# Kernel tuning notes

Measured on AMD Instinct MI355X. Metric: run time of the kernel, lower is better.

## Reference

```python
import jax, jax.numpy as jnp
import numpy as np

B, T, D, H = 32, 1024, 256, 256


def setup_inputs() -> dict:
    key = jax.random.key(0)
    ks = jax.random.split(key, 11)
    x = jax.random.normal(ks[0], (B, T, D), dtype=jnp.float32)
    len_x = jax.random.randint(ks[1], (B,), 1, T + 1).astype(jnp.int32)

    def xavier(k, fan_in, fan_out):
        return (jax.random.normal(k, (fan_out, fan_in)) * np.sqrt(2.0 / (fan_in + fan_out))).astype(jnp.float32)

    def unif(k, fan_in, shape):
        bound = 1.0 / np.sqrt(fan_in)
        return jax.random.uniform(k, shape, minval=-bound, maxval=bound).astype(jnp.float32)

    return {
        "x": x, "len_x": len_x,
        "Ww1_w": xavier(ks[2], D, H), "Ww1_b": unif(ks[3], D, (H,)),
        "Ww2_w": unif(ks[4], H, (D, H)), "Ww2_b": unif(ks[5], H, (D,)),
        "Wb1_w": xavier(ks[6], D, H), "Wb1_b": unif(ks[7], D, (H,)),
        "Wb2_w": unif(ks[8], H, (D, H)), "Wb2_b": unif(ks[9], H, (D,)),
    }


def _mlp(c, w1, b1, w2, b2):
    h = jax.nn.gelu(c @ w1.T + b1, approximate=False)
    return h @ w2.T + b2


def _ragged_dft(z, lengths, inverse):
    # z: [B, T, D] complex64; per-sample DFT over the first lengths[i] steps.
    t = z.shape[1]
    n = jnp.arange(t)
    kn = (n[:, None] * n[None, :]).astype(jnp.float32)          # [T, T]
    l = lengths.astype(jnp.float32)[:, None, None]               # [B, 1, 1]
    sign = 1.0 if inverse else -1.0
    ang = sign * 2.0 * jnp.pi * kn[None, :, :] / l               # [B, T, T]
    valid = n[None, :] < lengths[:, None]                        # [B, T]
    mask = (valid[:, :, None] & valid[:, None, :]).astype(jnp.float32)
    Wm = jnp.exp(1j * ang).astype(jnp.complex64) * mask
    if inverse:
        Wm = Wm / l.astype(jnp.complex64)
    return jnp.einsum("bkn,bnd->bkd", Wm, z)


def _crelu(z):
    mag = jnp.abs(z)
    phase = jnp.angle(z)
    recomposed = (mag * jnp.exp(1j * phase)).astype(jnp.complex64)
    return jnp.where(mag > 0, recomposed, jnp.zeros((), jnp.complex64))


def reference(x, len_x, Ww1_w, Ww1_b, Ww2_w, Ww2_b, Wb1_w, Wb1_b, Wb2_w, Wb2_b):
    # mean over valid length (torch sums over full T; padding assumed zero-filled contributes)
    c = jnp.sum(x, axis=1) / len_x.astype(x.dtype)[:, None]      # [B, D]
    x_freq = _ragged_dft(x.astype(jnp.complex64), len_x, inverse=False)
    W = _mlp(c, Ww1_w, Ww1_b, Ww2_w, Ww2_b).astype(jnp.complex64)  # [B, D]
    b = _mlp(c, Wb1_w, Wb1_b, Wb2_w, Wb2_b).astype(jnp.complex64)  # [B, D]
    filtered = x_freq * (1.0 + W[:, None, :]) + b[:, None, :]
    activated = _crelu(filtered)
    x_recon = _ragged_dft(activated, len_x, inverse=True)
    return x_recon.real.astype(x.dtype)
```

## Files before the change

### kernel.cpp

```cpp
#include <hip/hip_runtime.h>
#include <math.h>

#define BB 32
#define TT 1024
#define DD 256
#define NCHUNK 16
#define TCH (TT / NCHUNK)

__global__ void k_partial(const float* __restrict__ x, float* __restrict__ partial) {
    int blk = blockIdx.x;
    int b   = blk / NCHUNK;
    int ch  = blk % NCHUNK;
    int d   = threadIdx.x;
    const float* px = x + ((size_t)b * TT + (size_t)ch * TCH) * DD + d;
    float s = 0.f;
#pragma unroll 8
    for (int t = 0; t < TCH; ++t) s += px[(size_t)t * DD];
    partial[(b * NCHUNK + ch) * DD + d] = s;
}

__global__ void k_cfinal(const float* __restrict__ partial, const int* __restrict__ len,
                         float* __restrict__ c) {
    int b = blockIdx.x;
    int d = threadIdx.x;
    float s = 0.f;
#pragma unroll
    for (int ch = 0; ch < NCHUNK; ++ch) s += partial[(b * NCHUNK + ch) * DD + d];
    c[b * DD + d] = s / (float)len[b];
}

__device__ __forceinline__ float wave_reduce(float s) {
#pragma unroll
    for (int off = 32; off; off >>= 1) s += __shfl_xor(s, off, 64);
    return s;
}

__global__ void k_layer1(const float* __restrict__ c,
                         const float* __restrict__ w1a, const float* __restrict__ b1a,
                         const float* __restrict__ w1b, const float* __restrict__ b1b,
                         float* __restrict__ h) {
    int gwave = (blockIdx.x * blockDim.x + threadIdx.x) >> 6;
    int lane  = threadIdx.x & 63;
    int mlp   = gwave >> 8;
    int j     = gwave & 255;
    const float* w1 = mlp ? w1b : w1a;
    const float* b1 = mlp ? b1b : b1a;
    float4 wr  = ((const float4*)(w1 + j * DD))[lane];
    float bias = b1[j];
    for (int b = 0; b < BB; ++b) {
        float4 cc = ((const float4*)(c + b * DD))[lane];
        float s = wr.x * cc.x + wr.y * cc.y + wr.z * cc.z + wr.w * cc.w;
        s = wave_reduce(s);
        if (lane == 0) {
            float v = s + bias;
            float g = 0.5f * v * (1.0f + erff(v * 0.70710678118654752440f));
            h[(mlp * BB + b) * DD + j] = g;
        }
    }
}

__global__ void k_layer2(const float* __restrict__ h,
                         const float* __restrict__ w2a, const float* __restrict__ b2a,
                         const float* __restrict__ w2b, const float* __restrict__ b2b,
                         float* __restrict__ Wout, float* __restrict__ Bout) {
    int gwave = (blockIdx.x * blockDim.x + threadIdx.x) >> 6;
    int lane  = threadIdx.x & 63;
    int mlp   = gwave >> 8;
    int d     = gwave & 255;
    const float* w2 = mlp ? w2b : w2a;
    const float* b2 = mlp ? b2b : b2a;
    float* outp = mlp ? Bout : Wout;
    float4 wr  = ((const float4*)(w2 + d * DD))[lane];
    float bias = b2[d];
    const float* hbase = h + mlp * BB * DD;
    for (int b = 0; b < BB; ++b) {
        float4 hh = ((const float4*)(hbase + b * DD))[lane];
        float s = wr.x * hh.x + wr.y * hh.y + wr.z * hh.z + wr.w * hh.w;
        s = wave_reduce(s);
        if (lane == 0) outp[b * DD + d] = s + bias;
    }
}

__global__ void k_apply(const float* __restrict__ x, const int* __restrict__ len,
                        const float* __restrict__ Wf, const float* __restrict__ Bf,
                        float* __restrict__ out) {
    int row  = blockIdx.x * 4 + (threadIdx.x >> 6);
    int lane = threadIdx.x & 63;
    int b = row >> 10;
    int t = row & 1023;
    int L = len[b];
    size_t base = (size_t)row * DD;
    float4* o4 = (float4*)(out + base);
    if (t >= L) {
        float4 z; z.x = 0.f; z.y = 0.f; z.z = 0.f; z.w = 0.f;
        o4[lane] = z;
        return;
    }
    float4 x4 = ((const float4*)(x + base))[lane];
    float4 w4 = ((const float4*)(Wf + b * DD))[lane];
    float4 r;
    r.x = x4.x + w4.x * x4.x;
    r.y = x4.y + w4.y * x4.y;
    r.z = x4.z + w4.z * x4.z;
    r.w = x4.w + w4.w * x4.w;
    if (t == 0) {
        float4 b4 = ((const float4*)(Bf + b * DD))[lane];
        r.x += b4.x; r.y += b4.y; r.z += b4.z; r.w += b4.w;
    }
    o4[lane] = r;
}

extern "C" void kernel_launch(void* const* d_in, const int* in_sizes, int n_in,
                              void* d_out, int out_size, void* d_ws, size_t ws_size,
                              hipStream_t stream) {
    const float* x     = (const float*)d_in[0];
    const int*   len   = (const int*)d_in[1];
    const float* Ww1_w = (const float*)d_in[2];
    const float* Ww1_b = (const float*)d_in[3];
    const float* Ww2_w = (const float*)d_in[4];
    const float* Ww2_b = (const float*)d_in[5];
    const float* Wb1_w = (const float*)d_in[6];
    const float* Wb1_b = (const float*)d_in[7];
    const float* Wb2_w = (const float*)d_in[8];
    const float* Wb2_b = (const float*)d_in[9];
    float* out = (float*)d_out;

    float* ws      = (float*)d_ws;
    float* partial = ws;
    float* c       = ws + 131072;
    float* h       = ws + 139264;
    float* Wout    = ws + 155648;
    float* Bout    = ws + 163840;

    k_partial<<<BB * NCHUNK, 256, 0, stream>>>(x, partial);
    k_cfinal<<<BB, 256, 0, stream>>>(partial, len, c);
    k_layer1<<<128, 256, 0, stream>>>(c, Ww1_w, Ww1_b, Wb1_w, Wb1_b, h);
    k_layer2<<<128, 256, 0, stream>>>(h, Ww2_w, Ww2_b, Wb2_w, Wb2_b, Wout, Bout);
    k_apply<<<BB * TT / 4, 256, 0, stream>>>(x, len, Wout, Bout, out);
}
```

Measured before the change: 139.6 us.

## Fuse all stages into one cooperative kernel with grid-wide syncs

Replaces the five separate launches (partial sums, mean, two MLP layers, apply) with a single cooperative kernel that uses grid.sync between phases. Each block reduces its 32 rows, then 64 blocks compute the per-batch MLPs in shared memory, and every block applies the result to the same rows it summed, so x can be reused from cache. This targets launch overhead and the second pass over x, at the cost of two grid-wide barriers and most blocks sitting idle during the MLP phase. It also needs all 1024 blocks resident at once for the cooperative launch.

```diff
diff --git a/kernel.cpp b/kernel.cpp
--- a/kernel.cpp
+++ b/kernel.cpp
@@ -1,113 +1,131 @@
 #include <hip/hip_runtime.h>
+#include <hip/hip_cooperative_groups.h>
 #include <math.h>
+
+namespace cg = cooperative_groups;
 
 #define BB 32
 #define TT 1024
 #define DD 256
-#define NCHUNK 16
-#define TCH (TT / NCHUNK)
+#define NBLK 1024
+#define ROWS_PER_BLK 32
+#define CHUNKS_PER_B 32
 
-__global__ void k_partial(const float* __restrict__ x, float* __restrict__ partial) {
-    int blk = blockIdx.x;
-    int b   = blk / NCHUNK;
-    int ch  = blk % NCHUNK;
-    int d   = threadIdx.x;
-    const float* px = x + ((size_t)b * TT + (size_t)ch * TCH) * DD + d;
-    float s = 0.f;
+__global__ __launch_bounds__(256, 4)
+void fused_all(const float* __restrict__ x, const int* __restrict__ len,
+               const float* __restrict__ Ww1_w, const float* __restrict__ Ww1_b,
+               const float* __restrict__ Ww2_w, const float* __restrict__ Ww2_b,
+               const float* __restrict__ Wb1_w, const float* __restrict__ Wb1_b,
+               const float* __restrict__ Wb2_w, const float* __restrict__ Wb2_b,
+               float* __restrict__ out,
+               float* __restrict__ partial,
+               float* __restrict__ Wout,
+               float* __restrict__ Bout)
+{
+    cg::grid_group grid = cg::this_grid();
+    __shared__ float4 red[4][64];
+    __shared__ float  csh[DD];
+    __shared__ float  hsh[DD];
+
+    const int g    = blockIdx.x;
+    const int tid  = threadIdx.x;
+    const int wave = tid >> 6;
+    const int lane = tid & 63;
+    const int row0 = g * ROWS_PER_BLK;
+
+    {
+        const float4* xr = (const float4*)(x + (size_t)(row0 + wave * 8) * DD);
+        float4 s; s.x = 0.f; s.y = 0.f; s.z = 0.f; s.w = 0.f;
+#pragma unroll
+        for (int r = 0; r < 8; ++r) {
+            float4 v = xr[(size_t)r * 64 + lane];
+            s.x += v.x; s.y += v.y; s.z += v.z; s.w += v.w;
+        }
+        red[wave][lane] = s;
+    }
+    __syncthreads();
+    if (tid < 64) {
+        float4 a = red[0][tid], b = red[1][tid], c = red[2][tid], d = red[3][tid];
+        float4 s;
+        s.x = (a.x + b.x) + (c.x + d.x);
+        s.y = (a.y + b.y) + (c.y + d.y);
+        s.z = (a.z + b.z) + (c.z + d.z);
+        s.w = (a.w + b.w) + (c.w + d.w);
+        ((float4*)(partial + (size_t)g * DD))[tid] = s;
+    }
+
+    grid.sync();
+
+    if (g < 2 * BB) {
+        const int b   = g >> 1;
+        const int mlp = g & 1;
+        {
+            float s = 0.f;
+            const float* pp = partial + (size_t)(b * CHUNKS_PER_B) * DD + tid;
+#pragma unroll
+            for (int ch = 0; ch < CHUNKS_PER_B; ++ch) s += pp[(size_t)ch * DD];
+            csh[tid] = s / (float)len[b];
+        }
+        __syncthreads();
+        const float* w1 = mlp ? Wb1_w : Ww1_w;
+        const float* b1 = mlp ? Wb1_b : Ww1_b;
+        const float* w2 = mlp ? Wb2_w : Ww2_w;
+        const float* b2 = mlp ? Wb2_b : Ww2_b;
+        float* op       = mlp ? Bout  : Wout;
+        {
+            const float4* wr = (const float4*)(w1 + (size_t)tid * DD);
+            const float4* cc = (const float4*)csh;
+            float s = 0.f;
 #pragma unroll 8
-    for (int t = 0; t < TCH; ++t) s += px[(size_t)t * DD];
-    partial[(b * NCHUNK + ch) * DD + d] = s;
-}
-
-__global__ void k_cfinal(const float* __restrict__ partial, const int* __restrict__ len,
-                         float* __restrict__ c) {
-    int b = blockIdx.x;
-    int d = threadIdx.x;
-    float s = 0.f;
-#pragma unroll
-    for (int ch = 0; ch < NCHUNK; ++ch) s += partial[(b * NCHUNK + ch) * DD + d];
-    c[b * DD + d] = s / (float)len[b];
-}
-
-__device__ __forceinline__ float wave_reduce(float s) {
-#pragma unroll
-    for (int off = 32; off; off >>= 1) s += __shfl_xor(s, off, 64);
-    return s;
-}
-
-__global__ void k_layer1(const float* __restrict__ c,
-                         const float* __restrict__ w1a, const float* __restrict__ b1a,
-                         const float* __restrict__ w1b, const float* __restrict__ b1b,
-                         float* __restrict__ h) {
-    int gwave = (blockIdx.x * blockDim.x + threadIdx.x) >> 6;
-    int lane  = threadIdx.x & 63;
-    int mlp   = gwave >> 8;
-    int j     = gwave & 255;
-    const float* w1 = mlp ? w1b : w1a;
-    const float* b1 = mlp ? b1b : b1a;
-    float4 wr  = ((const float4*)(w1 + j * DD))[lane];
-    float bias = b1[j];
-    for (int b = 0; b < BB; ++b) {
-        float4 cc = ((const float4*)(c + b * DD))[lane];
-        float s = wr.x * cc.x + wr.y * cc.y + wr.z * cc.z + wr.w * cc.w;
-        s = wave_reduce(s);
-        if (lane == 0) {
-            float v = s + bias;
-            float g = 0.5f * v * (1.0f + erff(v * 0.70710678118654752440f));
-            h[(mlp * BB + b) * DD + j] = g;
+            for (int k = 0; k < 64; ++k) {
+                float4 w = wr[k];
+                float4 c4 = cc[k];
+                s += w.x * c4.x + w.y * c4.y + w.z * c4.z + w.w * c4.w;
+            }
+            float v = s + b1[tid];
+            hsh[tid] = 0.5f * v * (1.0f + erff(v * 0.70710678118654752440f));
+        }
+        __syncthreads();
+        {
+            const float4* wr = (const float4*)(w2 + (size_t)tid * DD);
+            const float4* hh = (const float4*)hsh;
+            float s = 0.f;
+#pragma unroll 8
+            for (int k = 0; k < 64; ++k) {
+                float4 w = wr[k];
+                float4 h4 = hh[k];
+                s += w.x * h4.x + w.y * h4.y + w.z * h4.z + w.w * h4.w;
+            }
+            op[b * DD + tid] = s + b2[tid];
         }
     }
-}
 
-__global__ void k_layer2(const float* __restrict__ h,
-                         const float* __restrict__ w2a, const float* __restrict__ b2a,
-                         const float* __restrict__ w2b, const float* __restrict__ b2b,
-                         float* __restrict__ Wout, float* __restrict__ Bout) {
-    int gwave = (blockIdx.x * blockDim.x + threadIdx.x) >> 6;
-    int lane  = threadIdx.x & 63;
-    int mlp   = gwave >> 8;
-    int d     = gwave & 255;
-    const float* w2 = mlp ? w2b : w2a;
-    const float* b2 = mlp ? b2b : b2a;
-    float* outp = mlp ? Bout : Wout;
-    float4 wr  = ((const float4*)(w2 + d * DD))[lane];
-    float bias = b2[d];
-    const float* hbase = h + mlp * BB * DD;
-    for (int b = 0; b < BB; ++b) {
-        float4 hh = ((const float4*)(hbase + b * DD))[lane];
-        float s = wr.x * hh.x + wr.y * hh.y + wr.z * hh.z + wr.w * hh.w;
-        s = wave_reduce(s);
-        if (lane == 0) outp[b * DD + d] = s + bias;
+    grid.sync();
+
+    {
+        const int b = row0 >> 10;
+        const int L = len[b];
+        const float4 w4 = ((const float4*)(Wout + b * DD))[lane];
+        const float4 b4 = ((const float4*)(Bout + b * DD))[lane];
+#pragma unroll
+        for (int r = 0; r < 8; ++r) {
+            const int row = row0 + wave * 8 + r;
+            const int t   = row & (TT - 1);
+            const size_t base = (size_t)row * DD;
+            float4 res;
+            if (t >= L) {
+                res.x = 0.f; res.y = 0.f; res.z = 0.f; res.w = 0.f;
+            } else {
+                float4 x4 = ((const float4*)(x + base))[lane];
+                res.x = x4.x + w4.x * x4.x;
+                res.y = x4.y + w4.y * x4.y;
+                res.z = x4.z + w4.z * x4.z;
+                res.w = x4.w + w4.w * x4.w;
+                if (t == 0) { res.x += b4.x; res.y += b4.y; res.z += b4.z; res.w += b4.w; }
+            }
+            ((float4*)(out + base))[lane] = res;
+        }
     }
-}
-
-__global__ void k_apply(const float* __restrict__ x, const int* __restrict__ len,
-                        const float* __restrict__ Wf, const float* __restrict__ Bf,
-                        float* __restrict__ out) {
-    int row  = blockIdx.x * 4 + (threadIdx.x >> 6);
-    int lane = threadIdx.x & 63;
-    int b = row >> 10;
-    int t = row & 1023;
-    int L = len[b];
-    size_t base = (size_t)row * DD;
-    float4* o4 = (float4*)(out + base);
-    if (t >= L) {
-        float4 z; z.x = 0.f; z.y = 0.f; z.z = 0.f; z.w = 0.f;
-        o4[lane] = z;
-        return;
-    }
-    float4 x4 = ((const float4*)(x + base))[lane];
-    float4 w4 = ((const float4*)(Wf + b * DD))[lane];
-    float4 r;
-    r.x = x4.x + w4.x * x4.x;
-    r.y = x4.y + w4.y * x4.y;
-    r.z = x4.z + w4.z * x4.z;
-    r.w = x4.w + w4.w * x4.w;
-    if (t == 0) {
-        float4 b4 = ((const float4*)(Bf + b * DD))[lane];
-        r.x += b4.x; r.y += b4.y; r.z += b4.z; r.w += b4.w;
-    }
-    o4[lane] = r;
 }
 
 extern "C" void kernel_launch(void* const* d_in, const int* in_sizes, int n_in,
@@ -127,14 +145,15 @@
 
     float* ws      = (float*)d_ws;
     float* partial = ws;
-    float* c       = ws + 131072;
-    float* h       = ws + 139264;
-    float* Wout    = ws + 155648;
-    float* Bout    = ws + 163840;
+    float* Wout    = ws + 262144;
+    float* Bout    = ws + 270336;
 
-    k_partial<<<BB * NCHUNK, 256, 0, stream>>>(x, partial);
-    k_cfinal<<<BB, 256, 0, stream>>>(partial, len, c);
-    k_layer1<<<128, 256, 0, stream>>>(c, Ww1_w, Ww1_b, Wb1_w, Wb1_b, h);
-    k_layer2<<<128, 256, 0, stream>>>(h, Ww2_w, Ww2_b, Wb2_w, Wb2_b, Wout, Bout);
-    k_apply<<<BB * TT / 4, 256, 0, stream>>>(x, len, Wout, Bout, out);
+    void* args[] = {
+        (void*)&x, (void*)&len,
+        (void*)&Ww1_w, (void*)&Ww1_b, (void*)&Ww2_w, (void*)&Ww2_b,
+        (void*)&Wb1_w, (void*)&Wb1_b, (void*)&Wb2_w, (void*)&Wb2_b,
+        (void*)&out, (void*)&partial, (void*)&Wout, (void*)&Bout,
+    };
+    hipLaunchCooperativeKernel((const void*)fused_all, dim3(NBLK), dim3(256),
+                               args, 0, stream);
 }
```

Measured after the change: 303.4 us. 117% more time.
